# Kernel optimization log

Hardware: AMD Instinct MI355X
Metric: run time of the kernel (lower is better)

Reference implementation:

```python
import jax, jax.numpy as jnp
import numpy as np

B, T, S, C, H = 2, 2048, 2048, 1024, 16
D = C // H  # head dim = 64


def setup_inputs() -> dict:
    key = jax.random.key(0)
    ks = jax.random.split(key, 6)
    sc = 1.0 / np.sqrt(C)
    return {
        "q": jax.random.normal(ks[0], (B, T, C), jnp.float32),
        "p": jax.random.normal(ks[1], (B, S, C), jnp.float32),
        "Wq": jax.random.normal(ks[2], (C, C), jnp.float32) * sc,
        "Wk": jax.random.normal(ks[3], (C, C), jnp.float32) * sc,
        "Wv": jax.random.normal(ks[4], (C, C), jnp.float32) * sc,
        "Wo": jax.random.normal(ks[5], (C, C), jnp.float32) * sc,
    }


def reference(q, p, Wq, Wk, Wv, Wo):
    # Linear projections (no bias: config.bias=True -> nn.Linear bias=False)
    qh = (q @ Wq).reshape(B, T, H, D)  # [B,T,H,D]
    kh = (p @ Wk).reshape(B, S, H, D)  # [B,S,H,D]
    vh = (p @ Wv).reshape(B, S, H, D)  # [B,S,H,D]
    scale = 1.0 / jnp.sqrt(jnp.asarray(D, qh.dtype))
    att = jnp.einsum('bthd,bshd->bhts', qh, kh) * scale  # [B,H,T,S]
    att = jax.nn.softmax(att, axis=-1)
    y = jnp.einsum('bhts,bshd->bthd', att, vh).reshape(B, T, C)
    y = y @ Wo  # c_proj, dropout p=0 (eval)
    return y
```

## Files before the change

### kernel.cpp

```cpp
#include <hip/hip_runtime.h>
#include <hip/hip_bf16.h>
#include <stdint.h>

#define T_LEN 2048
#define CDIM  1024

typedef short bf16x8_t  __attribute__((ext_vector_type(8)));
typedef float f32x4_t   __attribute__((ext_vector_type(4)));
typedef float f32x16_t  __attribute__((ext_vector_type(16)));

__device__ __forceinline__ float fexp2(float x) {
  float r;
  asm("v_exp_f32 %0, %1" : "=v"(r) : "v"(x));
  return r;
}

__device__ __forceinline__ void gload_lds16(const void* gptr, void* lptr) {
  __builtin_amdgcn_global_load_lds(
      (const __attribute__((address_space(1))) unsigned int*)(gptr),
      (__attribute__((address_space(3))) unsigned int*)(lptr),
      16, 0, 0);
}

__device__ __forceinline__ unsigned short f2bf(float f) {
  union { float f; unsigned int u; } v; v.f = f;
  unsigned int u = v.u;
  return (unsigned short)((u + 0x7fffu + ((u >> 16) & 1u)) >> 16);
}

__device__ __forceinline__ unsigned int pk_bf16(float lo, float hi) {
  unsigned int r;
  asm("v_cvt_pk_bf16_f32 %0, %1, %2" : "=v"(r) : "v"(lo), "v"(hi));
  return r;
}
__device__ __forceinline__ unsigned short bf1(float v) {
  return (unsigned short)pk_bf16(v, v);
}

__global__ __launch_bounds__(256) void cast2_f32_bf16(const float* __restrict__ x0,
                                                      const float* __restrict__ x1,
                                                      unsigned short* __restrict__ y0,
                                                      unsigned short* __restrict__ y1) {
  int i = blockIdx.x * 256 + threadIdx.x;
  const float* x = blockIdx.y ? x1 : x0;
  unsigned short* y = blockIdx.y ? y1 : y0;
  const float4* x4 = (const float4*)x;
  float4 a = x4[i * 2], b = x4[i * 2 + 1];
  union { unsigned short u[8]; uint4 v; } o;
  o.u[0] = f2bf(a.x); o.u[1] = f2bf(a.y); o.u[2] = f2bf(a.z); o.u[3] = f2bf(a.w);
  o.u[4] = f2bf(b.x); o.u[5] = f2bf(b.y); o.u[6] = f2bf(b.z); o.u[7] = f2bf(b.w);
  ((uint4*)y)[i] = o.v;
}

__global__ __launch_bounds__(256) void transpose_cast4(const float* __restrict__ W0,
                                                       const float* __restrict__ W1,
                                                       const float* __restrict__ W2,
                                                       const float* __restrict__ W3,
                                                       unsigned short* __restrict__ Wall,
                                                       unsigned short* __restrict__ Wot) {
  __shared__ float tile[32][33];
  int z = blockIdx.z;
  const float* W = (z == 0) ? W0 : (z == 1) ? W1 : (z == 2) ? W2 : W3;
  unsigned short* Wt = (z < 3) ? (Wall + (size_t)z * 1024 * 1024) : Wot;
  int tx = threadIdx.x & 31, ty = threadIdx.x >> 5;
  int n0 = blockIdx.x * 32, k0 = blockIdx.y * 32;
#pragma unroll
  for (int i = 0; i < 4; ++i) {
    int r = ty + i * 8;
    tile[r][tx] = W[(size_t)(k0 + r) * CDIM + n0 + tx];
  }
  __syncthreads();
#pragma unroll
  for (int i = 0; i < 4; ++i) {
    int r = ty + i * 8;
    Wt[(size_t)(n0 + r) * CDIM + k0 + tx] = f2bf(tile[tx][r]);
  }
}

__global__ __launch_bounds__(256) void gemm_qkv(const unsigned short* __restrict__ qbm,
                                                const unsigned short* __restrict__ pbm,
                                                const unsigned short* __restrict__ Wall,
                                                unsigned short* __restrict__ Qh,
                                                unsigned short* __restrict__ Kh,
                                                unsigned short* __restrict__ Vt) {
  __shared__ unsigned short ldsA[2][128 * 64];
  __shared__ unsigned short ldsB[2][128 * 64];
  const int tid = threadIdx.x, lane = tid & 63, w = tid >> 6;
  const int wr = w >> 1, wc = w & 1;
  const int nblk = blockIdx.x % 24, mblk = blockIdx.x / 24;
  const int m0 = mblk * 128;
  const int n0 = nblk * 128;
  const char* Ab = (const char*)((nblk < 8) ? qbm : pbm);
  const char* Bb = (const char*)Wall;
  f32x4_t acc[4][4] = {};

  auto stage = [&](int buf, int kt) {
#pragma unroll
    for (int it = 0; it < 4; ++it) {
      int ob = it * 4096 + w * 1024;
      int o = ob + lane * 16;
      int row = o >> 7, cin = o & 127;
      int cs = cin ^ ((row & 7) << 4);
      gload_lds16(Ab + (size_t)(m0 + row) * 2048 + kt * 128 + cs, (char*)ldsA[buf] + ob);
      gload_lds16(Bb + (size_t)(n0 + row) * 2048 + kt * 128 + cs, (char*)ldsB[buf] + ob);
    }
  };

  stage(0, 0);
  __syncthreads();
  int cur = 0;
  for (int kt = 0; kt < 16; ++kt) {
    if (kt < 15) stage(cur ^ 1, kt + 1);
    const char* lA = (const char*)ldsA[cur];
    const char* lB = (const char*)ldsB[cur];
#pragma unroll
    for (int kf = 0; kf < 2; ++kf) {
      int c = kf * 64 + ((lane >> 4) << 4);
      bf16x8_t af[4], bfr[4];
#pragma unroll
      for (int mf = 0; mf < 4; ++mf) {
        int row = wr * 64 + mf * 16 + (lane & 15);
        af[mf] = *(const bf16x8_t*)(lA + row * 128 + (c ^ ((row & 7) << 4)));
      }
#pragma unroll
      for (int nf = 0; nf < 4; ++nf) {
        int row = wc * 64 + nf * 16 + (lane & 15);
        bfr[nf] = *(const bf16x8_t*)(lB + row * 128 + (c ^ ((row & 7) << 4)));
      }
      __builtin_amdgcn_s_setprio(1);
#pragma unroll
      for (int mf = 0; mf < 4; ++mf)
#pragma unroll
        for (int nf = 0; nf < 4; ++nf)
          acc[mf][nf] = __builtin_amdgcn_mfma_f32_16x16x32_bf16(af[mf], bfr[nf], acc[mf][nf], 0, 0, 0);
      __builtin_amdgcn_s_setprio(0);
    }
    __syncthreads();
    cur ^= 1;
  }

  const float oscale = (nblk < 8) ? 0.18033688011112042f : 1.0f;
#pragma unroll
  for (int mf = 0; mf < 4; ++mf)
#pragma unroll
    for (int nf = 0; nf < 4; ++nf)
#pragma unroll
      for (int j = 0; j < 4; ++j) {
        int row = m0 + wr * 64 + mf * 16 + ((lane >> 4) << 2) + j;
        int col = n0 + wc * 64 + nf * 16 + (lane & 15);
        float v = acc[mf][nf][j] * oscale;
        int b = row >> 11, ts = row & 2047;
        if (col < 1024) {
          int h = col >> 6, d = col & 63;
          Qh[(((size_t)(b * 16 + h)) * 2048 + ts) * 64 + d] = bf1(v);
        } else if (col < 2048) {
          int cc = col - 1024, h = cc >> 6, d = cc & 63;
          Kh[(((size_t)(b * 16 + h)) * 2048 + ts) * 64 + d] = bf1(v);
        } else {
          int cc = col - 2048, h = cc >> 6, d = cc & 63;
          Vt[(((size_t)(b * 16 + h)) * 64 + d) * 2048 + ts] = bf1(v);
        }
      }
}

__global__ __launch_bounds__(256) void gemm_out(const unsigned short* __restrict__ A,
                                                const unsigned short* __restrict__ Bt,
                                                float* __restrict__ Out) {
  __shared__ unsigned short ldsA[2][128 * 64];
  __shared__ unsigned short ldsB[2][64 * 64];
  const int tid = threadIdx.x, lane = tid & 63, w = tid >> 6;
  const int m0 = (blockIdx.x >> 4) * 128;
  const int n0 = (blockIdx.x & 15) * 64;
  const char* Ab = (const char*)A;
  const char* Bb = (const char*)Bt;
  f32x4_t acc[2][4] = {};

  auto stage = [&](int buf, int kt) {
#pragma unroll
    for (int it = 0; it < 4; ++it) {
      int ob = it * 4096 + w * 1024;
      int o = ob + lane * 16;
      int row = o >> 7, cin = o & 127;
      int cs = cin ^ ((row & 7) << 4);
      gload_lds16(Ab + (size_t)(m0 + row) * 2048 + kt * 128 + cs, (char*)ldsA[buf] + ob);
    }
#pragma unroll
    for (int it = 0; it < 2; ++it) {
      int ob = it * 4096 + w * 1024;
      int o = ob + lane * 16;
      int row = o >> 7, cin = o & 127;
      int cs = cin ^ ((row & 7) << 4);
      gload_lds16(Bb + (size_t)(n0 + row) * 2048 + kt * 128 + cs, (char*)ldsB[buf] + ob);
    }
  };

  stage(0, 0);
  __syncthreads();
  int cur = 0;
  for (int kt = 0; kt < 16; ++kt) {
    if (kt < 15) stage(cur ^ 1, kt + 1);
    const char* lA = (const char*)ldsA[cur];
    const char* lB = (const char*)ldsB[cur];
#pragma unroll
    for (int kf = 0; kf < 2; ++kf) {
      int c = kf * 64 + ((lane >> 4) << 4);
      bf16x8_t af[2], bfr[4];
#pragma unroll
      for (int mf = 0; mf < 2; ++mf) {
        int row = w * 32 + mf * 16 + (lane & 15);
        af[mf] = *(const bf16x8_t*)(lA + row * 128 + (c ^ ((row & 7) << 4)));
      }
#pragma unroll
      for (int nf = 0; nf < 4; ++nf) {
        int row = nf * 16 + (lane & 15);
        bfr[nf] = *(const bf16x8_t*)(lB + row * 128 + (c ^ ((row & 7) << 4)));
      }
      __builtin_amdgcn_s_setprio(1);
#pragma unroll
      for (int mf = 0; mf < 2; ++mf)
#pragma unroll
        for (int nf = 0; nf < 4; ++nf)
          acc[mf][nf] = __builtin_amdgcn_mfma_f32_16x16x32_bf16(af[mf], bfr[nf], acc[mf][nf], 0, 0, 0);
      __builtin_amdgcn_s_setprio(0);
    }
    __syncthreads();
    cur ^= 1;
  }

#pragma unroll
  for (int mf = 0; mf < 2; ++mf)
#pragma unroll
    for (int nf = 0; nf < 4; ++nf)
#pragma unroll
      for (int j = 0; j < 4; ++j) {
        int row = m0 + w * 32 + mf * 16 + ((lane >> 4) << 2) + j;
        int col = n0 + nf * 16 + (lane & 15);
        Out[(size_t)row * 1024 + col] = acc[mf][nf][j];
      }
}

template <int SPLIT>
__global__ __launch_bounds__(256) void attn32(const unsigned short* __restrict__ Qg,
                                              const unsigned short* __restrict__ Kg,
                                              const unsigned short* __restrict__ Vtg,
                                              unsigned short* __restrict__ Ag,
                                              float* __restrict__ OpA,
                                              float* __restrict__ OpB,
                                              float* __restrict__ Lp) {
  __shared__ unsigned short ldsK[2][64 * 64];
  __shared__ unsigned short ldsV[2][64 * 64];
  const int tid = threadIdx.x, lane = tid & 63, w = tid >> 6;
  const int hi = lane >> 5, ql = lane & 31;
  const int bh = blockIdx.y;
  const int q0 = blockIdx.x * 128 + w * 32;
  const int z = (SPLIT > 1) ? blockIdx.z : 0;
  const int sBeg = z * (2048 / SPLIT), sEnd = sBeg + 2048 / SPLIT;

  bf16x8_t qf[4];
#pragma unroll
  for (int kd = 0; kd < 4; ++kd)
    qf[kd] = *(const bf16x8_t*)(Qg + ((size_t)bh * T_LEN + q0 + ql) * 64 + kd * 16 + hi * 8);

  bf16x8_t ones;
#pragma unroll
  for (int i = 0; i < 8; ++i) ones[i] = (short)0x3F80;

  f32x16_t oacc[2] = {};
  f32x16_t lacc = {};

  const char* Kb = (const char*)(Kg + (size_t)bh * 2048 * 64);
  const char* Vb = (const char*)(Vtg + (size_t)bh * 64 * 2048);

  auto stage = [&](int buf, int s0) {
#pragma unroll
    for (int it = 0; it < 2; ++it) {
      int ob = it * 4096 + w * 1024;
      int o = ob + lane * 16;
      int row = o >> 7, cin = o & 127;
      int cs = cin ^ ((row & 7) << 4);
      gload_lds16(Kb + (size_t)s0 * 128 + row * 128 + cs, (char*)ldsK[buf] + ob);
      gload_lds16(Vb + (size_t)s0 * 2 + (size_t)row * 4096 + cs, (char*)ldsV[buf] + ob);
    }
  };

  stage(0, sBeg);
  __syncthreads();
  int cur = 0;

  for (int s0 = sBeg; s0 < sEnd; s0 += 64) {
    if (s0 + 64 < sEnd) stage(cur ^ 1, s0 + 64);
    const char* lK = (const char*)ldsK[cur];
    const char* lV = (const char*)ldsV[cur];

    f32x16_t sacc[2] = {};
    __builtin_amdgcn_s_setprio(1);
#pragma unroll
    for (int sub = 0; sub < 2; ++sub) {
      int row = sub * 32 + ql;
      int swz = (row & 7) << 4;
#pragma unroll
      for (int kd = 0; kd < 4; ++kd) {
        bf16x8_t kfrag = *(const bf16x8_t*)(lK + row * 128 + ((kd * 32 + hi * 16) ^ swz));
        sacc[sub] = __builtin_amdgcn_mfma_f32_32x32x16_bf16(kfrag, qf[kd], sacc[sub], 0, 0, 0);
      }
    }
    __builtin_amdgcn_s_setprio(0);

#pragma unroll
    for (int sub = 0; sub < 2; ++sub)
#pragma unroll
      for (int r = 0; r < 16; ++r) sacc[sub][r] = fexp2(sacc[sub][r]);

#pragma unroll
    for (int ks = 0; ks < 4; ++ks) {
      const int sub = ks >> 1, mA = (ks & 1) * 2, mB = mA + 1;
      unsigned int a0 = pk_bf16(sacc[sub][4 * mA + 0], sacc[sub][4 * mA + 1]);
      unsigned int a1 = pk_bf16(sacc[sub][4 * mA + 2], sacc[sub][4 * mA + 3]);
      unsigned int b0 = pk_bf16(sacc[sub][4 * mB + 0], sacc[sub][4 * mB + 1]);
      unsigned int b1 = pk_bf16(sacc[sub][4 * mB + 2], sacc[sub][4 * mB + 3]);
      asm("v_permlane32_swap_b32 %0, %1" : "+v"(a0), "+v"(b0));
      asm("v_permlane32_swap_b32 %0, %1" : "+v"(a1), "+v"(b1));
      union { unsigned int u[4]; bf16x8_t v; } P;
      P.u[0] = a0; P.u[1] = a1; P.u[2] = b0; P.u[3] = b1;
      __builtin_amdgcn_s_setprio(1);
      lacc = __builtin_amdgcn_mfma_f32_32x32x16_bf16(P.v, ones, lacc, 0, 0, 0);
#pragma unroll
      for (int dt = 0; dt < 2; ++dt) {
        int row = dt * 32 + ql;
        bf16x8_t vfrag = *(const bf16x8_t*)(lV + row * 128 + ((ks * 32 + hi * 16) ^ ((row & 7) << 4)));
        oacc[dt] = __builtin_amdgcn_mfma_f32_32x32x16_bf16(P.v, vfrag, oacc[dt], 0, 0, 0);
      }
      __builtin_amdgcn_s_setprio(0);
    }
    __syncthreads();
    cur ^= 1;
  }

  const int b = bh >> 4, h = bh & 15;
  if (SPLIT == 1) {
#pragma unroll
    for (int grp = 0; grp < 4; ++grp)
#pragma unroll
      for (int r2 = 0; r2 < 4; ++r2) {
        int reg = grp * 4 + r2;
        float linv = 1.0f / lacc[reg];
        int t = q0 + 4 * hi + 8 * grp + r2;
#pragma unroll
        for (int dt = 0; dt < 2; ++dt) {
          int col = h * 64 + dt * 32 + ql;
          float v = oacc[dt][reg] * linv;
          Ag[((size_t)b * T_LEN + t) * CDIM + col] = bf1(v);
        }
      }
  } else {
    float* Op = (SPLIT == 4) ? (OpA + (size_t)z * 4194304) : (z ? OpB : OpA);
#pragma unroll
    for (int grp = 0; grp < 4; ++grp)
#pragma unroll
      for (int r2 = 0; r2 < 4; ++r2) {
        int reg = grp * 4 + r2;
        int t = q0 + 4 * hi + 8 * grp + r2;
#pragma unroll
        for (int dt = 0; dt < 2; ++dt)
          Op[((size_t)b * T_LEN + t) * CDIM + h * 64 + dt * 32 + ql] = oacc[dt][reg];
        if (ql == 0)
          Lp[(((size_t)z * 2 + b) * 16 + h) * T_LEN + t] = lacc[reg];
      }
  }
}

__global__ __launch_bounds__(256) void attn_combine(const float* __restrict__ O0,
                                                    const float* __restrict__ O1,
                                                    const float* __restrict__ Lp,
                                                    unsigned short* __restrict__ Ag) {
  int i = blockIdx.x * 256 + threadIdx.x;
  int c8 = i & 127, bt = i >> 7;
  int b = bt >> 11, t = bt & 2047;
  int c = c8 * 8, h = c >> 6;
  float l0 = Lp[(((size_t)0 * 2 + b) * 16 + h) * T_LEN + t];
  float l1 = Lp[(((size_t)1 * 2 + b) * 16 + h) * T_LEN + t];
  float inv = 1.0f / (l0 + l1);
  size_t off = (size_t)bt * CDIM + c;
  float4 x0 = *(const float4*)(O0 + off);
  float4 x1 = *(const float4*)(O1 + off);
  float4 y0 = *(const float4*)(O0 + off + 4);
  float4 y1 = *(const float4*)(O1 + off + 4);
  union { unsigned int u[4]; uint4 v; } o;
  o.u[0] = pk_bf16((x0.x + x1.x) * inv, (x0.y + x1.y) * inv);
  o.u[1] = pk_bf16((x0.z + x1.z) * inv, (x0.w + x1.w) * inv);
  o.u[2] = pk_bf16((y0.x + y1.x) * inv, (y0.y + y1.y) * inv);
  o.u[3] = pk_bf16((y0.z + y1.z) * inv, (y0.w + y1.w) * inv);
  *(uint4*)(Ag + off) = o.v;
}

__global__ __launch_bounds__(256) void attn_combine4(const float* __restrict__ Op,
                                                     const float* __restrict__ Lp,
                                                     unsigned short* __restrict__ Ag) {
  int i = blockIdx.x * 256 + threadIdx.x;
  int c8 = i & 127, bt = i >> 7;
  int b = bt >> 11, t = bt & 2047;
  int c = c8 * 8, h = c >> 6;
  float l = 0.f;
#pragma unroll
  for (int z = 0; z < 4; ++z)
    l += Lp[(((size_t)z * 2 + b) * 16 + h) * T_LEN + t];
  float inv = 1.0f / l;
  size_t off = (size_t)bt * CDIM + c;
  float s[8] = {0, 0, 0, 0, 0, 0, 0, 0};
#pragma unroll
  for (int z = 0; z < 4; ++z) {
    const float* P = Op + (size_t)z * 4194304 + off;
    float4 x = *(const float4*)P;
    float4 y = *(const float4*)(P + 4);
    s[0] += x.x; s[1] += x.y; s[2] += x.z; s[3] += x.w;
    s[4] += y.x; s[5] += y.y; s[6] += y.z; s[7] += y.w;
  }
  union { unsigned int u[4]; uint4 v; } o;
  o.u[0] = pk_bf16(s[0] * inv, s[1] * inv);
  o.u[1] = pk_bf16(s[2] * inv, s[3] * inv);
  o.u[2] = pk_bf16(s[4] * inv, s[5] * inv);
  o.u[3] = pk_bf16(s[6] * inv, s[7] * inv);
  *(uint4*)(Ag + off) = o.v;
}

extern "C" void kernel_launch(void* const* d_in, const int* in_sizes, int n_in,
                              void* d_out, int out_size, void* d_ws, size_t ws_size,
                              hipStream_t stream) {
  const float* q  = (const float*)d_in[0];
  const float* p  = (const float*)d_in[1];
  const float* Wq = (const float*)d_in[2];
  const float* Wk = (const float*)d_in[3];
  const float* Wv = (const float*)d_in[4];
  const float* Wo = (const float*)d_in[5];

  char* ws = (char*)d_ws;
  const size_t MB = (size_t)1 << 20;
  unsigned short* qb   = (unsigned short*)(ws);
  unsigned short* pb   = (unsigned short*)(ws + 8 * MB);
  unsigned short* Wall = (unsigned short*)(ws + 16 * MB);
  unsigned short* Wot  = (unsigned short*)(ws + 22 * MB);
  unsigned short* Qh   = (unsigned short*)(ws + 24 * MB);
  unsigned short* Kh   = (unsigned short*)(ws + 32 * MB);
  unsigned short* Vt   = (unsigned short*)(ws + 40 * MB);
  unsigned short* Ao   = (unsigned short*)(ws + 48 * MB);

  cast2_f32_bf16<<<dim3(2048, 2), 256, 0, stream>>>(q, p, qb, pb);
  transpose_cast4<<<dim3(32, 32, 4), 256, 0, stream>>>(Wq, Wk, Wv, Wo, Wall, Wot);

  gemm_qkv<<<768, 256, 0, stream>>>(qb, pb, Wall, Qh, Kh, Vt);

  if (ws_size >= 121 * MB) {
    float* OpBase = (float*)(ws + 56 * MB);
    float* Lp4    = (float*)(ws + 120 * MB);
    attn32<4><<<dim3(16, 32, 4), 256, 0, stream>>>(Qh, Kh, Vt, nullptr, OpBase, nullptr, Lp4);
    attn_combine4<<<2048, 256, 0, stream>>>(OpBase, Lp4, Ao);
  } else if (ws_size >= 73 * MB) {
    float* O0 = (float*)(ws);
    float* O1 = (float*)(ws + 56 * MB);
    float* Lp = (float*)(ws + 72 * MB);
    attn32<2><<<dim3(16, 32, 2), 256, 0, stream>>>(Qh, Kh, Vt, nullptr, O0, O1, Lp);
    attn_combine<<<2048, 256, 0, stream>>>(O0, O1, Lp, Ao);
  } else {
    attn32<1><<<dim3(16, 32, 1), 256, 0, stream>>>(Qh, Kh, Vt, Ao, nullptr, nullptr, nullptr);
  }

  gemm_out<<<512, 256, 0, stream>>>(Ao, Wot, (float*)d_out);
}
```

Before: 154.7 us.

## Software-pipeline QK^T of the next tile with PV of the current tile, drop split-4

```diff
diff --git a/kernel.cpp b/kernel.cpp
--- a/kernel.cpp
+++ b/kernel.cpp
@@ -240,21 +240,22 @@
 }
 
 template <int SPLIT>
-__global__ __launch_bounds__(256) void attn32(const unsigned short* __restrict__ Qg,
-                                              const unsigned short* __restrict__ Kg,
-                                              const unsigned short* __restrict__ Vtg,
-                                              unsigned short* __restrict__ Ag,
-                                              float* __restrict__ OpA,
-                                              float* __restrict__ OpB,
-                                              float* __restrict__ Lp) {
-  __shared__ unsigned short ldsK[2][64 * 64];
+__global__ __launch_bounds__(256, 3) void attn32(const unsigned short* __restrict__ Qg,
+                                                 const unsigned short* __restrict__ Kg,
+                                                 const unsigned short* __restrict__ Vtg,
+                                                 unsigned short* __restrict__ Ag,
+                                                 float* __restrict__ OpA,
+                                                 float* __restrict__ OpB,
+                                                 float* __restrict__ Lp) {
+  __shared__ unsigned short ldsK[3][64 * 64];
   __shared__ unsigned short ldsV[2][64 * 64];
   const int tid = threadIdx.x, lane = tid & 63, w = tid >> 6;
   const int hi = lane >> 5, ql = lane & 31;
   const int bh = blockIdx.y;
   const int q0 = blockIdx.x * 128 + w * 32;
   const int z = (SPLIT > 1) ? blockIdx.z : 0;
-  const int sBeg = z * (2048 / SPLIT), sEnd = sBeg + 2048 / SPLIT;
+  constexpr int NT = 2048 / SPLIT / 64;
+  const int sBeg = z * (2048 / SPLIT);
 
   bf16x8_t qf[4];
 #pragma unroll
@@ -267,33 +268,36 @@
 
   f32x16_t oacc[2] = {};
   f32x16_t lacc = {};
+  const f32x16_t vzero = {};
 
   const char* Kb = (const char*)(Kg + (size_t)bh * 2048 * 64);
   const char* Vb = (const char*)(Vtg + (size_t)bh * 64 * 2048);
 
-  auto stage = [&](int buf, int s0) {
+  auto stageK = [&](int slot, int t) {
+    int s0 = sBeg + t * 64;
 #pragma unroll
     for (int it = 0; it < 2; ++it) {
       int ob = it * 4096 + w * 1024;
       int o = ob + lane * 16;
       int row = o >> 7, cin = o & 127;
       int cs = cin ^ ((row & 7) << 4);
-      gload_lds16(Kb + (size_t)s0 * 128 + row * 128 + cs, (char*)ldsK[buf] + ob);
-      gload_lds16(Vb + (size_t)s0 * 2 + (size_t)row * 4096 + cs, (char*)ldsV[buf] + ob);
-    }
-  };
-
-  stage(0, sBeg);
-  __syncthreads();
-  int cur = 0;
-
-  for (int s0 = sBeg; s0 < sEnd; s0 += 64) {
-    if (s0 + 64 < sEnd) stage(cur ^ 1, s0 + 64);
-    const char* lK = (const char*)ldsK[cur];
-    const char* lV = (const char*)ldsV[cur];
-
-    f32x16_t sacc[2] = {};
-    __builtin_amdgcn_s_setprio(1);
+      gload_lds16(Kb + (size_t)s0 * 128 + row * 128 + cs, (char*)ldsK[slot] + ob);
+    }
+  };
+  auto stageV = [&](int slot, int t) {
+    int s0 = sBeg + t * 64;
+#pragma unroll
+    for (int it = 0; it < 2; ++it) {
+      int ob = it * 4096 + w * 1024;
+      int o = ob + lane * 16;
+      int row = o >> 7, cin = o & 127;
+      int cs = cin ^ ((row & 7) << 4);
+      gload_lds16(Vb + (size_t)s0 * 2 + (size_t)row * 4096 + cs, (char*)ldsV[slot] + ob);
+    }
+  };
+
+  auto qk = [&](f32x16_t (&s)[2], int slot) {
+    const char* lK = (const char*)ldsK[slot];
 #pragma unroll
     for (int sub = 0; sub < 2; ++sub) {
       int row = sub * 32 + ql;
@@ -301,28 +305,26 @@
 #pragma unroll
       for (int kd = 0; kd < 4; ++kd) {
         bf16x8_t kfrag = *(const bf16x8_t*)(lK + row * 128 + ((kd * 32 + hi * 16) ^ swz));
-        sacc[sub] = __builtin_amdgcn_mfma_f32_32x32x16_bf16(kfrag, qf[kd], sacc[sub], 0, 0, 0);
-      }
-    }
-    __builtin_amdgcn_s_setprio(0);
-
-#pragma unroll
-    for (int sub = 0; sub < 2; ++sub)
-#pragma unroll
-      for (int r = 0; r < 16; ++r) sacc[sub][r] = fexp2(sacc[sub][r]);
-
+        s[sub] = __builtin_amdgcn_mfma_f32_32x32x16_bf16(kfrag, qf[kd], s[sub], 0, 0, 0);
+      }
+    }
+  };
+
+  auto consume = [&](f32x16_t (&s)[2], int vslot) {
+    const char* lV = (const char*)ldsV[vslot];
 #pragma unroll
     for (int ks = 0; ks < 4; ++ks) {
       const int sub = ks >> 1, mA = (ks & 1) * 2, mB = mA + 1;
-      unsigned int a0 = pk_bf16(sacc[sub][4 * mA + 0], sacc[sub][4 * mA + 1]);
-      unsigned int a1 = pk_bf16(sacc[sub][4 * mA + 2], sacc[sub][4 * mA + 3]);
-      unsigned int b0 = pk_bf16(sacc[sub][4 * mB + 0], sacc[sub][4 * mB + 1]);
-      unsigned int b1 = pk_bf16(sacc[sub][4 * mB + 2], sacc[sub][4 * mB + 3]);
+      float e0 = fexp2(s[sub][4 * mA + 0]), e1 = fexp2(s[sub][4 * mA + 1]);
+      float e2 = fexp2(s[sub][4 * mA + 2]), e3 = fexp2(s[sub][4 * mA + 3]);
+      float e4 = fexp2(s[sub][4 * mB + 0]), e5 = fexp2(s[sub][4 * mB + 1]);
+      float e6 = fexp2(s[sub][4 * mB + 2]), e7 = fexp2(s[sub][4 * mB + 3]);
+      unsigned int a0 = pk_bf16(e0, e1), a1 = pk_bf16(e2, e3);
+      unsigned int b0 = pk_bf16(e4, e5), b1 = pk_bf16(e6, e7);
       asm("v_permlane32_swap_b32 %0, %1" : "+v"(a0), "+v"(b0));
       asm("v_permlane32_swap_b32 %0, %1" : "+v"(a1), "+v"(b1));
       union { unsigned int u[4]; bf16x8_t v; } P;
       P.u[0] = a0; P.u[1] = a1; P.u[2] = b0; P.u[3] = b1;
-      __builtin_amdgcn_s_setprio(1);
       lacc = __builtin_amdgcn_mfma_f32_32x32x16_bf16(P.v, ones, lacc, 0, 0, 0);
 #pragma unroll
       for (int dt = 0; dt < 2; ++dt) {
@@ -330,10 +332,29 @@
         bf16x8_t vfrag = *(const bf16x8_t*)(lV + row * 128 + ((ks * 32 + hi * 16) ^ ((row & 7) << 4)));
         oacc[dt] = __builtin_amdgcn_mfma_f32_32x32x16_bf16(P.v, vfrag, oacc[dt], 0, 0, 0);
       }
-      __builtin_amdgcn_s_setprio(0);
-    }
+    }
+  };
+
+  f32x16_t sA[2] = {}, sB[2] = {};
+  stageK(0, 0);
+  stageV(0, 0);
+  stageK(1, 1);
+  __syncthreads();
+  qk(sA, 0);
+
+  for (int i = 0; i < NT; i += 2) {
+    if (i + 2 < NT) stageK((i + 2) % 3, i + 2);
+    if (i + 1 < NT) stageV((i + 1) & 1, i + 1);
+    if (i + 1 < NT) { sB[0] = vzero; sB[1] = vzero; qk(sB, (i + 1) % 3); }
+    consume(sA, i & 1);
     __syncthreads();
-    cur ^= 1;
+    if (i + 1 < NT) {
+      if (i + 3 < NT) stageK((i + 3) % 3, i + 3);
+      if (i + 2 < NT) stageV((i + 2) & 1, i + 2);
+      if (i + 2 < NT) { sA[0] = vzero; sA[1] = vzero; qk(sA, (i + 2) % 3); }
+      consume(sB, (i + 1) & 1);
+      __syncthreads();
+    }
   }
 
   const int b = bh >> 4, h = bh & 15;
@@ -353,7 +374,7 @@
         }
       }
   } else {
-    float* Op = (SPLIT == 4) ? (OpA + (size_t)z * 4194304) : (z ? OpB : OpA);
+    float* Op = z ? OpB : OpA;
 #pragma unroll
     for (int grp = 0; grp < 4; ++grp)
 #pragma unroll
@@ -393,36 +414,6 @@
   *(uint4*)(Ag + off) = o.v;
 }
 
-__global__ __launch_bounds__(256) void attn_combine4(const float* __restrict__ Op,
-                                                     const float* __restrict__ Lp,
-                                                     unsigned short* __restrict__ Ag) {
-  int i = blockIdx.x * 256 + threadIdx.x;
-  int c8 = i & 127, bt = i >> 7;
-  int b = bt >> 11, t = bt & 2047;
-  int c = c8 * 8, h = c >> 6;
-  float l = 0.f;
-#pragma unroll
-  for (int z = 0; z < 4; ++z)
-    l += Lp[(((size_t)z * 2 + b) * 16 + h) * T_LEN + t];
-  float inv = 1.0f / l;
-  size_t off = (size_t)bt * CDIM + c;
-  float s[8] = {0, 0, 0, 0, 0, 0, 0, 0};
-#pragma unroll
-  for (int z = 0; z < 4; ++z) {
-    const float* P = Op + (size_t)z * 4194304 + off;
-    float4 x = *(const float4*)P;
-    float4 y = *(const float4*)(P + 4);
-    s[0] += x.x; s[1] += x.y; s[2] += x.z; s[3] += x.w;
-    s[4] += y.x; s[5] += y.y; s[6] += y.z; s[7] += y.w;
-  }
-  union { unsigned int u[4]; uint4 v; } o;
-  o.u[0] = pk_bf16(s[0] * inv, s[1] * inv);
-  o.u[1] = pk_bf16(s[2] * inv, s[3] * inv);
-  o.u[2] = pk_bf16(s[4] * inv, s[5] * inv);
-  o.u[3] = pk_bf16(s[6] * inv, s[7] * inv);
-  *(uint4*)(Ag + off) = o.v;
-}
-
 extern "C" void kernel_launch(void* const* d_in, const int* in_sizes, int n_in,
                               void* d_out, int out_size, void* d_ws, size_t ws_size,
                               hipStream_t stream) {
@@ -449,12 +440,7 @@
 
   gemm_qkv<<<768, 256, 0, stream>>>(qb, pb, Wall, Qh, Kh, Vt);
 
-  if (ws_size >= 121 * MB) {
-    float* OpBase = (float*)(ws + 56 * MB);
-    float* Lp4    = (float*)(ws + 120 * MB);
-    attn32<4><<<dim3(16, 32, 4), 256, 0, stream>>>(Qh, Kh, Vt, nullptr, OpBase, nullptr, Lp4);
-    attn_combine4<<<2048, 256, 0, stream>>>(OpBase, Lp4, Ao);
-  } else if (ws_size >= 73 * MB) {
+  if (ws_size >= 73 * MB) {
     float* O0 = (float*)(ws);
     float* O1 = (float*)(ws + 56 * MB);
     float* Lp = (float*)(ws + 72 * MB);
```

Measured after the change: 148.1 us. -4.2%, faster.
